# Performance work log

Measured on AMD Instinct MI355X. Metric: run time of the kernel, lower is better.

## Reference

```python
import jax, jax.numpy as jnp
import numpy as np

B, L, D, S = 4, 4096, 1024, 16
EPS = 1e-5  # nn.LayerNorm default


def setup_inputs() -> dict:
    key = jax.random.key(0)
    ks = jax.random.split(key, 8)
    s = 0.02
    return {
        "x_seq": jax.random.normal(ks[0], (B, L, D), jnp.float32),
        "h_prev": jnp.zeros((B, S), jnp.float32),
        "gamma": jnp.ones((D,), jnp.float32),
        "beta": jnp.zeros((D,), jnp.float32),
        "W_in": jax.random.normal(ks[1], (D, D), jnp.float32) * s,
        "b_in": jnp.zeros((D,), jnp.float32),
        "W_A": jax.random.normal(ks[2], (D, S), jnp.float32) * s,
        "b_A": jnp.zeros((S,), jnp.float32),
        "W_B": jax.random.normal(ks[3], (D, S), jnp.float32) * s,
        "b_B": jnp.zeros((S,), jnp.float32),
        "W_C": jax.random.normal(ks[4], (D, S), jnp.float32) * s,
        "b_C": jnp.zeros((S,), jnp.float32),
        "W_dt": jax.random.normal(ks[5], (D, 1), jnp.float32) * s,
        "b_dt": jnp.zeros((1,), jnp.float32),
        "W_out": jax.random.normal(ks[6], (D, D), jnp.float32) * s,
        "b_out": jnp.zeros((D,), jnp.float32),
    }


def _layernorm(x, gamma, beta):
    mu = jnp.mean(x, axis=-1, keepdims=True)
    var = jnp.mean(jnp.square(x - mu), axis=-1, keepdims=True)
    return (x - mu) * jax.lax.rsqrt(var + EPS) * gamma + beta


def reference(x_seq, h_prev, gamma, beta, W_in, b_in, W_A, b_A, W_B, b_B,
              W_C, b_C, W_dt, b_dt, W_out, b_out):
    # pre-scan projections (all batched over (B, L))
    x = _layernorm(x_seq, gamma, beta)
    x = jax.nn.silu(x @ W_in + b_in)                    # (B, L, D)
    log_A = -jax.nn.softplus(x @ W_A + b_A)             # (B, L, S)
    B_t = x @ W_B + b_B                                 # (B, L, S)
    C_t = x @ W_C + b_C                                 # (B, L, S)
    dt = jax.nn.softplus(x @ W_dt + b_dt)               # (B, L, 1)
    A_disc = jnp.exp(log_A * dt)                        # (B, L, S)
    u = jnp.mean(x, axis=-1, keepdims=True)             # (B, L, 1)
    Bu = (B_t * dt) * u                                 # (B, L, S)

    # selective scan: h_t = A_t * h_{t-1} + Bu_t  over time axis
    def step(h, inp):
        a_t, bu_t = inp
        h = a_t * h + bu_t
        return h, h

    h_final, hs = jax.lax.scan(
        step, h_prev,
        (jnp.swapaxes(A_disc, 0, 1), jnp.swapaxes(Bu, 0, 1)))
    hs = jnp.swapaxes(hs, 0, 1)                         # (B, L, S)

    y = jnp.sum(C_t * hs, axis=-1, keepdims=True)       # (B, L, 1)
    y_seq = (x * y) @ W_out + b_out + x_seq             # (B, L, D)
    return y_seq, h_final
```

## Files before the change

kernel.cpp:

```cpp
#include <hip/hip_runtime.h>

typedef unsigned short u16;
typedef unsigned int u32;
typedef __attribute__((ext_vector_type(8))) short short8;
typedef __attribute__((ext_vector_type(4))) float f32x4;

#define B_ 4
#define L_ 4096
#define D_ 1024
#define S_ 16
#define M_ (B_ * L_)
#define NBG 64
#define LC 64

__device__ __forceinline__ float b2f(u16 h) {
    unsigned u = ((unsigned)h) << 16;
    return __builtin_bit_cast(float, u);
}
__device__ __forceinline__ u16 f2b(float f) {
    unsigned u = __builtin_bit_cast(unsigned, f);
    u += 0x7fffu + ((u >> 16) & 1u);
    return (u16)(u >> 16);
}
__device__ __forceinline__ float softplus_f(float z) {
    return z > 20.f ? z : log1pf(__expf(z));
}
__device__ __forceinline__ void gload16(const u16* g, const u16* l) {
    __builtin_amdgcn_global_load_lds(
        (const __attribute__((address_space(1))) u32*)g,
        (__attribute__((address_space(3))) u32*)l, 16, 0, 0);
}

__global__ __launch_bounds__(256) void prep_kernel(
    const float* __restrict__ W0, u16* __restrict__ Wt0,
    const float* __restrict__ W1, u16* __restrict__ Wt1,
    const float* __restrict__ WA, const float* __restrict__ WB,
    const float* __restrict__ WC, const float* __restrict__ Wdt,
    u16* __restrict__ Wp) {
    int b = blockIdx.x, tid = threadIdx.x;
    if (b < 2048) {
        const float* W = (b >> 10) ? W1 : W0;
        u16* Wt = (b >> 10) ? Wt1 : Wt0;
        int by = (b >> 5) & 31, bx = b & 31;
        int x = tid & 31, ty = tid >> 5;
        __shared__ float t[32][33];
        for (int j = ty; j < 32; j += 8)
            t[j][x] = W[(size_t)(by * 32 + j) * D_ + bx * 32 + x];
        __syncthreads();
        for (int j = ty; j < 32; j += 8)
            Wt[(size_t)(bx * 32 + j) * D_ + by * 32 + x] = f2b(t[x][j]);
    } else {
        int idx = (b - 2048) * 256 + tid;
        int s = idx >> 10, k = idx & 1023;
        float v;
        if (s < 16)       v = WA[k * 16 + s];
        else if (s < 32)  v = WB[k * 16 + (s - 16)];
        else if (s < 48)  v = WC[k * 16 + (s - 32)];
        else if (s == 48) v = Wdt[k];
        else if (s == 49) v = 1.0f / 1024.0f;
        else              v = 0.f;
        Wp[idx] = f2b(v);
    }
}

__global__ __launch_bounds__(256) void ln_kernel(
    const float* __restrict__ x, const float* __restrict__ gamma,
    const float* __restrict__ beta, u16* __restrict__ out) {
    int row = blockIdx.x, tid = threadIdx.x;
    const float4 v = *(const float4*)&x[(size_t)row * D_ + tid * 4];
    float s = v.x + v.y + v.z + v.w;
    float q = v.x * v.x + v.y * v.y + v.z * v.z + v.w * v.w;
    for (int o = 32; o > 0; o >>= 1) { s += __shfl_down(s, o); q += __shfl_down(q, o); }
    __shared__ float ss[4], qq[4];
    int w = tid >> 6, lane = tid & 63;
    if (lane == 0) { ss[w] = s; qq[w] = q; }
    __syncthreads();
    if (tid == 0) {
        float S = ss[0] + ss[1] + ss[2] + ss[3];
        float Q = qq[0] + qq[1] + qq[2] + qq[3];
        float mu = S * (1.f / D_);
        float var = Q * (1.f / D_) - mu * mu;
        ss[0] = mu; qq[0] = rsqrtf(var + 1e-5f);
    }
    __syncthreads();
    float mu = ss[0], rs = qq[0];
    const float4 gv = *(const float4*)&gamma[tid * 4];
    const float4 bv = *(const float4*)&beta[tid * 4];
    ushort4 o4;
    o4.x = f2b((v.x - mu) * rs * gv.x + bv.x);
    o4.y = f2b((v.y - mu) * rs * gv.y + bv.y);
    o4.z = f2b((v.z - mu) * rs * gv.z + bv.z);
    o4.w = f2b((v.w - mu) * rs * gv.w + bv.w);
    *(ushort4*)&out[(size_t)row * D_ + tid * 4] = o4;
}

template <int EPI>
__global__ __launch_bounds__(512, 1) void gemm256(
    const u16* __restrict__ A, const u16* __restrict__ Bt,
    const float* __restrict__ bias, const float* __restrict__ resid,
    const float* __restrict__ yrow,
    u16* __restrict__ outB, float* __restrict__ outF,
    int M, int N, int K, int nTileN) {
    __shared__ u16 sm[65536];
    const int TILES = K >> 6;

    int nwg = gridDim.x;
    int bid = blockIdx.x;
    int swz = (bid & 7) * (nwg >> 3) + (bid >> 3);
    int bx = swz % nTileN, by = swz / nTileN;
    int rowBase = by * 256, colBase = bx * 256;

    int tid = threadIdx.x;
    int lane = tid & 63, w = tid >> 6;
    int wr = w >> 2, wc = w & 3;
    int lr = lane & 15, lg = lane >> 4;
    const unsigned woff = (unsigned)((lr * 32 + lg * 8) ^ ((lr & 8) ? 16 : 0));

    int sub = w;
    int pos = sub >> 1;
    int kblk = sub & 1;
    int r = lane >> 2;
    int chunk = (lane & 3) ^ ((r & 8) ? 2 : 0);
    int rowoff = (pos & 1) * 16 + (pos >> 1) * 128;
    const u16* gAs = A  + (size_t)(rowBase + rowoff + r) * K + kblk * 32 + chunk * 8;
    const u16* gBs = Bt + (size_t)(colBase + rowoff + r) * K + kblk * 32 + chunk * 8;
    const unsigned subb = (unsigned)sub * 512u;

#define STAGEPAIR(tau, p)                                                        \
    do {                                                                         \
        unsigned _bb = (unsigned)((tau) & 1) * 32768u;                           \
        size_t _go = (size_t)(p) * 32 * K + (size_t)(tau) * 64;                  \
        gload16(gBs + _go, &sm[_bb + 16384u + (unsigned)(p) * 4096u + subb]);    \
        gload16(gAs + _go, &sm[_bb + (unsigned)(p) * 4096u + subb]);             \
    } while (0)

    f32x4 acc[8][4] = {};

    STAGEPAIR(0, 0); STAGEPAIR(0, 1); STAGEPAIR(0, 2); STAGEPAIR(0, 3);
    if (TILES > 1) { STAGEPAIR(1, 0); STAGEPAIR(1, 1); STAGEPAIR(1, 2); }
    asm volatile("s_waitcnt vmcnt(6)" ::: "memory");
    __builtin_amdgcn_s_barrier();

    for (int t = 0; t < TILES; ++t) {
        const unsigned bb = (unsigned)(t & 1) * 32768u;
        short8 bfr[4][2], afr[2][2];
        if (t + 1 < TILES) STAGEPAIR(t + 1, 3);
#pragma unroll
        for (int n = 0; n < 4; n++) {
            int rb = wc * 4 + n;
            unsigned bo = bb + 16384u + (unsigned)(((rb & 7) >> 1)) * 4096u
                        + (unsigned)(((rb & 1) + ((rb >> 3) << 1)) << 1) * 512u + woff;
            bfr[n][0] = *(const short8*)&sm[bo];
            bfr[n][1] = *(const short8*)&sm[bo + 512u];
        }
#pragma unroll
        for (int dm = 0; dm < 2; dm++) {
            unsigned ao = bb + (unsigned)((dm + (wr << 1)) << 1) * 512u + woff;
            afr[dm][0] = *(const short8*)&sm[ao];
            afr[dm][1] = *(const short8*)&sm[ao + 512u];
        }
        __builtin_amdgcn_s_barrier();
        __builtin_amdgcn_s_setprio(1);
#pragma unroll
        for (int dm = 0; dm < 2; dm++)
#pragma unroll
            for (int n = 0; n < 4; n++)
#pragma unroll
                for (int ks = 0; ks < 2; ks++)
                    acc[dm][n] = __builtin_amdgcn_mfma_f32_16x16x32_bf16(
                        afr[dm][ks], bfr[n][ks], acc[dm][n], 0, 0, 0);
        __builtin_amdgcn_s_setprio(0);
        __builtin_amdgcn_s_barrier();
#pragma unroll
        for (int q = 1; q < 4; q++) {
            if (t + 2 < TILES) STAGEPAIR(t + 2, q - 1);
#pragma unroll
            for (int dm = 0; dm < 2; dm++) {
                int m = q * 2 + dm;
                unsigned ao = bb + (unsigned)q * 4096u
                            + (unsigned)(((m & 1) + (wr << 1)) << 1) * 512u + woff;
                afr[dm][0] = *(const short8*)&sm[ao];
                afr[dm][1] = *(const short8*)&sm[ao + 512u];
            }
            __builtin_amdgcn_s_barrier();
            __builtin_amdgcn_s_setprio(1);
#pragma unroll
            for (int dm = 0; dm < 2; dm++)
#pragma unroll
                for (int n = 0; n < 4; n++)
#pragma unroll
                    for (int ks = 0; ks < 2; ks++)
                        acc[q * 2 + dm][n] = __builtin_amdgcn_mfma_f32_16x16x32_bf16(
                            afr[dm][ks], bfr[n][ks], acc[q * 2 + dm][n], 0, 0, 0);
            __builtin_amdgcn_s_setprio(0);
            if (q == 3) {
                if (t + 2 < TILES)      asm volatile("s_waitcnt vmcnt(6)" ::: "memory");
                else if (t + 1 < TILES) asm volatile("s_waitcnt vmcnt(0)" ::: "memory");
            }
            __builtin_amdgcn_s_barrier();
        }
    }
#undef STAGEPAIR

    if (EPI == 1) {
        float bcol[4];
#pragma unroll
        for (int n = 0; n < 4; n++) bcol[n] = bias[colBase + wc * 64 + n * 16 + lr];
#pragma unroll
        for (int m = 0; m < 8; m++)
#pragma unroll
            for (int n = 0; n < 4; n++)
#pragma unroll
                for (int j = 0; j < 4; j++) {
                    int row = wr * 128 + m * 16 + lg * 4 + j;
                    int col = wc * 64 + n * 16 + lr;
                    float v = acc[m][n][j] + bcol[n];
                    v = v / (1.f + __expf(-v));
                    int cbs = (col >> 4) ^ lg;
                    sm[row * 256 + cbs * 16 + (col & 15)] = f2b(v);
                }
        __syncthreads();
        int rr = tid >> 1, half = tid & 1;
        u16* gout = outB + (size_t)(rowBase + rr) * N + colBase;
#pragma unroll
        for (int q = 0; q < 8; q++) {
            int cb = half * 8 + q;
            int cbs = cb ^ ((rr >> 2) & 3);
            *(uint4*)&gout[cb * 16] = *(const uint4*)&sm[rr * 256 + cbs * 16];
        }
    } else {
        float bcol[4];
#pragma unroll
        for (int n = 0; n < 4; n++) bcol[n] = bias[colBase + wc * 64 + n * 16 + lr];
#pragma unroll
        for (int m = 0; m < 8; m++) {
            float yr[4];
#pragma unroll
            for (int j = 0; j < 4; j++)
                yr[j] = yrow[rowBase + wr * 128 + m * 16 + lg * 4 + j];
#pragma unroll
            for (int n = 0; n < 4; n++)
#pragma unroll
                for (int j = 0; j < 4; j++) {
                    int row = rowBase + wr * 128 + m * 16 + lg * 4 + j;
                    int col = colBase + wc * 64 + n * 16 + lr;
                    size_t o = (size_t)row * N + col;
                    outF[o] = acc[m][n][j] * yr[j] + bcol[n] + resid[o];
                }
        }
    }
}

__global__ __launch_bounds__(256) void proj_kernel(
    const u16* __restrict__ X, const u16* __restrict__ Wp,
    const float* __restrict__ bA, const float* __restrict__ bB,
    const float* __restrict__ bC, const float* __restrict__ bdt,
    float* __restrict__ Ad, float* __restrict__ Bu, float* __restrict__ Ct) {
    __shared__ u16 Xs[2][64][32];
    __shared__ u16 Ws[2][64][32];
    int rowBase = blockIdx.x * 64;
    int tid = threadIdx.x, lane = tid & 63, w = tid >> 6;
    int lr = lane & 15, lg = lane >> 4;
    f32x4 acc[4] = {};
    const int sr = lane >> 2, sc = (lane & 3) * 8;
    const u16* gX = &X[(size_t)(rowBase + w * 16 + sr) * 1024 + sc];
    const u16* gW = &Wp[(size_t)(w * 16 + sr) * 1024 + sc];

#define PSTAGE(d, k0)                              \
    do {                                           \
        gload16(gX + (k0), &Xs[d][w * 16][0]);     \
        gload16(gW + (k0), &Ws[d][w * 16][0]);     \
    } while (0)

    PSTAGE(0, 0);
    __syncthreads();
    int cur = 0;
    for (int k0 = 0; k0 < 1024; k0 += 32) {
        if (k0 + 32 < 1024) PSTAGE(cur ^ 1, k0 + 32);
        short8 a = *(const short8*)&Xs[cur][w * 16 + lr][lg * 8];
#pragma unroll
        for (int n = 0; n < 4; n++) {
            short8 b = *(const short8*)&Ws[cur][n * 16 + lr][lg * 8];
            acc[n] = __builtin_amdgcn_mfma_f32_16x16x32_bf16(a, b, acc[n], 0, 0, 0);
        }
        __syncthreads();
        cur ^= 1;
    }
#undef PSTAGE
    float bdt0 = bdt[0];
#pragma unroll
    for (int j = 0; j < 4; j++) {
        int row = rowBase + w * 16 + lg * 4 + j;
        float dtr = __shfl(acc[3][j], lg * 16 + 0, 64);
        float uv  = __shfl(acc[3][j], lg * 16 + 1, 64);
        float dt = softplus_f(dtr + bdt0);
        float zA = acc[0][j] + bA[lr];
        float zB = acc[1][j] + bB[lr];
        float zC = acc[2][j] + bC[lr];
        size_t o = (size_t)row * 16 + lr;
        Ad[o] = __expf(-dt * softplus_f(zA));
        Bu[o] = zB * dt * uv;
        Ct[o] = zC;
    }
}

__global__ __launch_bounds__(1024) void scan_part1(
    const float* __restrict__ Ad, const float* __restrict__ Bu,
    float* __restrict__ Pb, float* __restrict__ Qb) {
    int b = blockIdx.x >> 6, g = blockIdx.x & 63;
    int tid = threadIdx.x;
    int s = tid & 15, c = tid >> 4;
    size_t idx = ((size_t)b * L_ + g * LC + c) * S_ + s;
    float a = Ad[idx], bu = Bu[idx];
    __shared__ float Ps[16][64], Qs[16][64];
    Ps[s][c] = a; Qs[s][c] = bu;
    __syncthreads();
    if (tid < 16) {
        float P = 1.f, Q = 0.f;
        for (int cc = 0; cc < 64; cc++) {
            float pa = Ps[tid][cc], qa = Qs[tid][cc];
            P = pa * P;
            Q = pa * Q + qa;
        }
        int o = (b * NBG + g) * S_ + tid;
        Pb[o] = P; Qb[o] = Q;
    }
}

__global__ __launch_bounds__(64) void scan_part2(
    const float* __restrict__ Pb, const float* __restrict__ Qb,
    const float* __restrict__ hprev, float* __restrict__ Hb,
    float* __restrict__ hfinal) {
    int t = threadIdx.x;
    int b = t >> 4, s = t & 15;
    float h = hprev[b * S_ + s];
    for (int g = 0; g < NBG; g++) {
        int o = (b * NBG + g) * S_ + s;
        Hb[o] = h;
        h = Pb[o] * h + Qb[o];
    }
    hfinal[b * S_ + s] = h;
}

__global__ __launch_bounds__(1024) void scan_part3(
    const float* __restrict__ Ad, const float* __restrict__ Bu,
    const float* __restrict__ Ct, const float* __restrict__ Hb,
    float* __restrict__ y) {
    int b = blockIdx.x >> 6, g = blockIdx.x & 63;
    int tid = threadIdx.x;
    int s = tid & 15, c = tid >> 4;
    size_t idx = ((size_t)b * L_ + g * LC + c) * S_ + s;
    float a = Ad[idx], bu = Bu[idx];
    __shared__ float Ps[16][64], Qs[16][64], Hin[16][65];
    Ps[s][c] = a; Qs[s][c] = bu;
    __syncthreads();
    if (tid < 16) {
        float h = Hb[(b * NBG + g) * S_ + tid];
        for (int cc = 0; cc < 64; cc++) {
            Hin[tid][cc] = h;
            h = Ps[tid][cc] * h + Qs[tid][cc];
        }
    }
    __syncthreads();
    float h = a * Hin[s][c] + bu;
    float p = Ct[idx] * h;
    p += __shfl_xor(p, 1);
    p += __shfl_xor(p, 2);
    p += __shfl_xor(p, 4);
    p += __shfl_xor(p, 8);
    if (s == 0) y[(size_t)b * L_ + g * LC + c] = p;
}

extern "C" void kernel_launch(void* const* d_in, const int* in_sizes, int n_in,
                              void* d_out, int out_size, void* d_ws, size_t ws_size,
                              hipStream_t stream) {
    const float* x_seq  = (const float*)d_in[0];
    const float* h_prev = (const float*)d_in[1];
    const float* gamma  = (const float*)d_in[2];
    const float* beta   = (const float*)d_in[3];
    const float* W_in   = (const float*)d_in[4];
    const float* b_in   = (const float*)d_in[5];
    const float* W_A    = (const float*)d_in[6];
    const float* b_A    = (const float*)d_in[7];
    const float* W_B    = (const float*)d_in[8];
    const float* b_B    = (const float*)d_in[9];
    const float* W_C    = (const float*)d_in[10];
    const float* b_C    = (const float*)d_in[11];
    const float* W_dt   = (const float*)d_in[12];
    const float* b_dt   = (const float*)d_in[13];
    const float* W_out  = (const float*)d_in[14];
    const float* b_out  = (const float*)d_in[15];

    char* ws = (char*)d_ws;
    u16*   x_ln   = (u16*)(ws + 0);
    u16*   x      = (u16*)(ws + 33554432);
    u16*   Wt_in  = (u16*)(ws + 67108864);
    u16*   Wt_out = (u16*)(ws + 69206016);
    u16*   Wp     = (u16*)(ws + 71303168);
    float* Ad     = (float*)(ws + 71434240);
    float* Bu     = (float*)(ws + 72482816);
    float* Ct     = (float*)(ws + 73531392);
    float* yv     = (float*)(ws + 74579968);
    float* Pb     = (float*)(ws + 74645504);
    float* Qb     = (float*)(ws + 74661888);
    float* Hb     = (float*)(ws + 74678272);
    float* out    = (float*)d_out;

    prep_kernel<<<2304, 256, 0, stream>>>(W_in, Wt_in, W_out, Wt_out,
                                          W_A, W_B, W_C, W_dt, Wp);
    ln_kernel<<<M_, 256, 0, stream>>>(x_seq, gamma, beta, x_ln);
    gemm256<1><<<(M_ / 256) * (D_ / 256), 512, 0, stream>>>(
        x_ln, Wt_in, b_in, nullptr, nullptr, x, nullptr, M_, D_, D_, D_ / 256);
    proj_kernel<<<M_ / 64, 256, 0, stream>>>(x, Wp, b_A, b_B, b_C, b_dt, Ad, Bu, Ct);
    scan_part1<<<B_ * NBG, 1024, 0, stream>>>(Ad, Bu, Pb, Qb);
    scan_part2<<<1, 64, 0, stream>>>(Pb, Qb, h_prev, Hb, out + (size_t)M_ * D_);
    scan_part3<<<B_ * NBG, 1024, 0, stream>>>(Ad, Bu, Ct, Hb, yv);
    gemm256<2><<<(M_ / 256) * (D_ / 256), 512, 0, stream>>>(
        x, Wt_out, b_out, x_seq, yv, nullptr, out, M_, D_, D_, D_ / 256);
}
```

Baseline: 153.3 us.

## Fuse LN with weight prep, and chunk scan into projection and scan kernels

Merges the layernorm and weight-prep kernels into one launch. Moves the per-chunk scan reduction (scan_part1) into the projection kernel's epilogue, using its 64-row tile as the chunk. Replaces the single-block carry scan (scan_part2) with each scan_part3 block recomputing its incoming carry serially from the chunk summaries. This drops three launches and one serial tiny kernel, at the cost of extra serial work per block (up to 63 steps) and a shared-memory reduction in the projection kernel.

```diff
diff --git a/kernel.cpp b/kernel.cpp
--- a/kernel.cpp
+++ b/kernel.cpp
@@ -31,26 +31,56 @@
         (__attribute__((address_space(3))) u32*)l, 16, 0, 0);
 }
 
-__global__ __launch_bounds__(256) void prep_kernel(
+__global__ __launch_bounds__(256) void ln_prep_kernel(
+    const float* __restrict__ x, const float* __restrict__ gamma,
+    const float* __restrict__ beta, u16* __restrict__ xout,
     const float* __restrict__ W0, u16* __restrict__ Wt0,
     const float* __restrict__ W1, u16* __restrict__ Wt1,
     const float* __restrict__ WA, const float* __restrict__ WB,
     const float* __restrict__ WC, const float* __restrict__ Wdt,
     u16* __restrict__ Wp) {
-    int b = blockIdx.x, tid = threadIdx.x;
-    if (b < 2048) {
+    int blk = blockIdx.x, tid = threadIdx.x;
+    if (blk < M_) {
+        int row = blk;
+        const float4 v = *(const float4*)&x[(size_t)row * D_ + tid * 4];
+        float s = v.x + v.y + v.z + v.w;
+        float q = v.x * v.x + v.y * v.y + v.z * v.z + v.w * v.w;
+        for (int o = 32; o > 0; o >>= 1) { s += __shfl_down(s, o); q += __shfl_down(q, o); }
+        __shared__ float ss[4], qq[4];
+        int w = tid >> 6, lane = tid & 63;
+        if (lane == 0) { ss[w] = s; qq[w] = q; }
+        __syncthreads();
+        if (tid == 0) {
+            float S = ss[0] + ss[1] + ss[2] + ss[3];
+            float Q = qq[0] + qq[1] + qq[2] + qq[3];
+            float mu = S * (1.f / D_);
+            float var = Q * (1.f / D_) - mu * mu;
+            ss[0] = mu; qq[0] = rsqrtf(var + 1e-5f);
+        }
+        __syncthreads();
+        float mu = ss[0], rs = qq[0];
+        const float4 gv = *(const float4*)&gamma[tid * 4];
+        const float4 bv = *(const float4*)&beta[tid * 4];
+        ushort4 o4;
+        o4.x = f2b((v.x - mu) * rs * gv.x + bv.x);
+        o4.y = f2b((v.y - mu) * rs * gv.y + bv.y);
+        o4.z = f2b((v.z - mu) * rs * gv.z + bv.z);
+        o4.w = f2b((v.w - mu) * rs * gv.w + bv.w);
+        *(ushort4*)&xout[(size_t)row * D_ + tid * 4] = o4;
+    } else if (blk < M_ + 2048) {
+        int b = blk - M_;
         const float* W = (b >> 10) ? W1 : W0;
         u16* Wt = (b >> 10) ? Wt1 : Wt0;
         int by = (b >> 5) & 31, bx = b & 31;
-        int x = tid & 31, ty = tid >> 5;
+        int xx = tid & 31, ty = tid >> 5;
         __shared__ float t[32][33];
         for (int j = ty; j < 32; j += 8)
-            t[j][x] = W[(size_t)(by * 32 + j) * D_ + bx * 32 + x];
+            t[j][xx] = W[(size_t)(by * 32 + j) * D_ + bx * 32 + xx];
         __syncthreads();
         for (int j = ty; j < 32; j += 8)
-            Wt[(size_t)(bx * 32 + j) * D_ + by * 32 + x] = f2b(t[x][j]);
+            Wt[(size_t)(bx * 32 + j) * D_ + by * 32 + xx] = f2b(t[xx][j]);
     } else {
-        int idx = (b - 2048) * 256 + tid;
+        int idx = (blk - M_ - 2048) * 256 + tid;
         int s = idx >> 10, k = idx & 1023;
         float v;
         if (s < 16)       v = WA[k * 16 + s];
@@ -61,37 +91,6 @@
         else              v = 0.f;
         Wp[idx] = f2b(v);
     }
-}
-
-__global__ __launch_bounds__(256) void ln_kernel(
-    const float* __restrict__ x, const float* __restrict__ gamma,
-    const float* __restrict__ beta, u16* __restrict__ out) {
-    int row = blockIdx.x, tid = threadIdx.x;
-    const float4 v = *(const float4*)&x[(size_t)row * D_ + tid * 4];
-    float s = v.x + v.y + v.z + v.w;
-    float q = v.x * v.x + v.y * v.y + v.z * v.z + v.w * v.w;
-    for (int o = 32; o > 0; o >>= 1) { s += __shfl_down(s, o); q += __shfl_down(q, o); }
-    __shared__ float ss[4], qq[4];
-    int w = tid >> 6, lane = tid & 63;
-    if (lane == 0) { ss[w] = s; qq[w] = q; }
-    __syncthreads();
-    if (tid == 0) {
-        float S = ss[0] + ss[1] + ss[2] + ss[3];
-        float Q = qq[0] + qq[1] + qq[2] + qq[3];
-        float mu = S * (1.f / D_);
-        float var = Q * (1.f / D_) - mu * mu;
-        ss[0] = mu; qq[0] = rsqrtf(var + 1e-5f);
-    }
-    __syncthreads();
-    float mu = ss[0], rs = qq[0];
-    const float4 gv = *(const float4*)&gamma[tid * 4];
-    const float4 bv = *(const float4*)&beta[tid * 4];
-    ushort4 o4;
-    o4.x = f2b((v.x - mu) * rs * gv.x + bv.x);
-    o4.y = f2b((v.y - mu) * rs * gv.y + bv.y);
-    o4.z = f2b((v.z - mu) * rs * gv.z + bv.z);
-    o4.w = f2b((v.w - mu) * rs * gv.w + bv.w);
-    *(ushort4*)&out[(size_t)row * D_ + tid * 4] = o4;
 }
 
 template <int EPI>
@@ -255,9 +254,11 @@
     const u16* __restrict__ X, const u16* __restrict__ Wp,
     const float* __restrict__ bA, const float* __restrict__ bB,
     const float* __restrict__ bC, const float* __restrict__ bdt,
-    float* __restrict__ Ad, float* __restrict__ Bu, float* __restrict__ Ct) {
+    float* __restrict__ Ad, float* __restrict__ Bu, float* __restrict__ Ct,
+    float* __restrict__ Pb, float* __restrict__ Qb) {
     __shared__ u16 Xs[2][64][32];
     __shared__ u16 Ws[2][64][32];
+    __shared__ float Psh[64][17], Qsh[64][17];
     int rowBase = blockIdx.x * 64;
     int tid = threadIdx.x, lane = tid & 63, w = tid >> 6;
     int lr = lane & 15, lg = lane >> 4;
@@ -290,7 +291,8 @@
     float bdt0 = bdt[0];
 #pragma unroll
     for (int j = 0; j < 4; j++) {
-        int row = rowBase + w * 16 + lg * 4 + j;
+        int rl = w * 16 + lg * 4 + j;
+        int row = rowBase + rl;
         float dtr = __shfl(acc[3][j], lg * 16 + 0, 64);
         float uv  = __shfl(acc[3][j], lg * 16 + 1, 64);
         float dt = softplus_f(dtr + bdt0);
@@ -298,54 +300,32 @@
         float zB = acc[1][j] + bB[lr];
         float zC = acc[2][j] + bC[lr];
         size_t o = (size_t)row * 16 + lr;
-        Ad[o] = __expf(-dt * softplus_f(zA));
-        Bu[o] = zB * dt * uv;
+        float adv = __expf(-dt * softplus_f(zA));
+        float buv = zB * dt * uv;
+        Ad[o] = adv;
+        Bu[o] = buv;
         Ct[o] = zC;
-    }
-}
-
-__global__ __launch_bounds__(1024) void scan_part1(
-    const float* __restrict__ Ad, const float* __restrict__ Bu,
-    float* __restrict__ Pb, float* __restrict__ Qb) {
-    int b = blockIdx.x >> 6, g = blockIdx.x & 63;
-    int tid = threadIdx.x;
-    int s = tid & 15, c = tid >> 4;
-    size_t idx = ((size_t)b * L_ + g * LC + c) * S_ + s;
-    float a = Ad[idx], bu = Bu[idx];
-    __shared__ float Ps[16][64], Qs[16][64];
-    Ps[s][c] = a; Qs[s][c] = bu;
+        Psh[rl][lr] = adv;
+        Qsh[rl][lr] = buv;
+    }
     __syncthreads();
     if (tid < 16) {
         float P = 1.f, Q = 0.f;
-        for (int cc = 0; cc < 64; cc++) {
-            float pa = Ps[tid][cc], qa = Qs[tid][cc];
+        for (int rr = 0; rr < 64; rr++) {
+            float pa = Psh[rr][tid];
             P = pa * P;
-            Q = pa * Q + qa;
-        }
-        int o = (b * NBG + g) * S_ + tid;
+            Q = pa * Q + Qsh[rr][tid];
+        }
+        int o = blockIdx.x * S_ + tid;
         Pb[o] = P; Qb[o] = Q;
     }
-}
-
-__global__ __launch_bounds__(64) void scan_part2(
-    const float* __restrict__ Pb, const float* __restrict__ Qb,
-    const float* __restrict__ hprev, float* __restrict__ Hb,
-    float* __restrict__ hfinal) {
-    int t = threadIdx.x;
-    int b = t >> 4, s = t & 15;
-    float h = hprev[b * S_ + s];
-    for (int g = 0; g < NBG; g++) {
-        int o = (b * NBG + g) * S_ + s;
-        Hb[o] = h;
-        h = Pb[o] * h + Qb[o];
-    }
-    hfinal[b * S_ + s] = h;
 }
 
 __global__ __launch_bounds__(1024) void scan_part3(
     const float* __restrict__ Ad, const float* __restrict__ Bu,
-    const float* __restrict__ Ct, const float* __restrict__ Hb,
-    float* __restrict__ y) {
+    const float* __restrict__ Ct, const float* __restrict__ Pb,
+    const float* __restrict__ Qb, const float* __restrict__ hprev,
+    float* __restrict__ y, float* __restrict__ hfinal) {
     int b = blockIdx.x >> 6, g = blockIdx.x & 63;
     int tid = threadIdx.x;
     int s = tid & 15, c = tid >> 4;
@@ -355,11 +335,16 @@
     Ps[s][c] = a; Qs[s][c] = bu;
     __syncthreads();
     if (tid < 16) {
-        float h = Hb[(b * NBG + g) * S_ + tid];
+        float h = hprev[b * S_ + tid];
+        for (int gg = 0; gg < g; gg++) {
+            int o = (b * NBG + gg) * S_ + tid;
+            h = Pb[o] * h + Qb[o];
+        }
         for (int cc = 0; cc < 64; cc++) {
             Hin[tid][cc] = h;
             h = Ps[tid][cc] * h + Qs[tid][cc];
         }
+        if (g == NBG - 1) hfinal[b * S_ + tid] = h;
     }
     __syncthreads();
     float h = a * Hin[s][c] + bu;
@@ -403,18 +388,17 @@
     float* yv     = (float*)(ws + 74579968);
     float* Pb     = (float*)(ws + 74645504);
     float* Qb     = (float*)(ws + 74661888);
-    float* Hb     = (float*)(ws + 74678272);
     float* out    = (float*)d_out;
 
-    prep_kernel<<<2304, 256, 0, stream>>>(W_in, Wt_in, W_out, Wt_out,
-                                          W_A, W_B, W_C, W_dt, Wp);
-    ln_kernel<<<M_, 256, 0, stream>>>(x_seq, gamma, beta, x_ln);
+    ln_prep_kernel<<<M_ + 2048 + 256, 256, 0, stream>>>(
+        x_seq, gamma, beta, x_ln,
+        W_in, Wt_in, W_out, Wt_out, W_A, W_B, W_C, W_dt, Wp);
     gemm256<1><<<(M_ / 256) * (D_ / 256), 512, 0, stream>>>(
         x_ln, Wt_in, b_in, nullptr, nullptr, x, nullptr, M_, D_, D_, D_ / 256);
-    proj_kernel<<<M_ / 64, 256, 0, stream>>>(x, Wp, b_A, b_B, b_C, b_dt, Ad, Bu, Ct);
-    scan_part1<<<B_ * NBG, 1024, 0, stream>>>(Ad, Bu, Pb, Qb);
-    scan_part2<<<1, 64, 0, stream>>>(Pb, Qb, h_prev, Hb, out + (size_t)M_ * D_);
-    scan_part3<<<B_ * NBG, 1024, 0, stream>>>(Ad, Bu, Ct, Hb, yv);
+    proj_kernel<<<M_ / 64, 256, 0, stream>>>(x, Wp, b_A, b_B, b_C, b_dt,
+                                             Ad, Bu, Ct, Pb, Qb);
+    scan_part3<<<B_ * NBG, 1024, 0, stream>>>(Ad, Bu, Ct, Pb, Qb, h_prev,
+                                              yv, out + (size_t)M_ * D_);
     gemm256<2><<<(M_ / 256) * (D_ / 256), 512, 0, stream>>>(
         x, Wt_out, b_out, x_seq, yv, nullptr, out, M_, D_, D_, D_ / 256);
 }
```

Result: no change. 152.0 us (-0.9%).
